# Kernel optimization log

Hardware: AMD Instinct MI355X
Metric: run time of the kernel (lower is better)

Reference implementation:

```python
import jax, jax.numpy as jnp
import numpy as np

N_NODES, N_EDGES, N_GRAPHS = 20000, 640000, 256
D_IN, H1, H2, H3, L, H4, ED = 7, 128, 128, 64, 16, 64, 1


def _gat_conv(x, src, dst, edge_attr, W, att_s, att_d, We, att_e, b):
    """PyG GATConv (heads=1, concat=True, edge_dim=ED, add_self_loops=True,
    fill_value='mean' for self-loop edge attrs, negative_slope=0.2)."""
    n = x.shape[0]
    h = x @ W                                  # [N, F]
    a_s = h @ att_s                            # [N]
    a_d = h @ att_d                            # [N]
    # append self loops; self-loop edge attr = mean of edge attrs
    loop = jnp.arange(n)
    src_f = jnp.concatenate([src, loop])
    dst_f = jnp.concatenate([dst, loop])
    ea_mean = edge_attr.mean(axis=0, keepdims=True)
    ea = jnp.concatenate([edge_attr, jnp.broadcast_to(ea_mean, (n, edge_attr.shape[1]))], axis=0)
    a_e = (ea @ We) @ att_e                    # [E+N]
    logits = jax.nn.leaky_relu(a_s[src_f] + a_d[dst_f] + a_e, 0.2)
    # neighborhood softmax over incoming edges of each dst node
    m = jax.ops.segment_max(logits, dst_f, num_segments=n)
    ex = jnp.exp(logits - m[dst_f])
    denom = jax.ops.segment_sum(ex, dst_f, num_segments=n)
    alpha = ex / denom[dst_f]                  # [E+N]
    out = jax.ops.segment_sum(alpha[:, None] * h[src_f], dst_f, num_segments=n)
    return out + b


def _branch(x, edge_index, edge_col, params):
    src, dst = edge_index[0], edge_index[1]
    for p in params:  # fixed 3 layers
        x = jax.nn.elu(_gat_conv(x, src, dst, edge_col, *p))
        # dropout p=0.2 is identity in eval mode
    return x


def _mean_pool(x, batch, num_graphs):
    s = jax.ops.segment_sum(x, batch, num_segments=num_graphs)
    cnt = jax.ops.segment_sum(jnp.ones((x.shape[0],), x.dtype), batch, num_segments=num_graphs)
    return s / jnp.maximum(cnt, 1.0)[:, None]


def setup_inputs() -> dict:
    key = jax.random.key(0)
    ks = jax.random.split(key, 40)
    inp = {
        "x1": jax.random.normal(ks[0], (N_NODES, D_IN), jnp.float32),
        "x2": jax.random.normal(ks[1], (N_NODES, D_IN), jnp.float32),
        "edge_index1": jax.random.randint(ks[2], (2, N_EDGES), 0, N_NODES),
        "edge_index2": jax.random.randint(ks[3], (2, N_EDGES), 0, N_NODES),
        "batch1": jnp.sort(jax.random.randint(ks[4], (N_NODES,), 0, N_GRAPHS)),
        "batch2": jnp.sort(jax.random.randint(ks[5], (N_NODES,), 0, N_GRAPHS)),
        "x_norm2_1": jax.random.normal(ks[6], (N_GRAPHS, L), jnp.float32),
        "x_norm2_2": jax.random.normal(ks[7], (N_GRAPHS, L), jnp.float32),
        "edge_col1": jax.random.normal(ks[8], (N_EDGES, ED), jnp.float32),
        "edge_col2": jax.random.normal(ks[9], (N_EDGES, ED), jnp.float32),
    }
    dims = [(D_IN, H1), (H1, H2), (H2, H3)]
    k = 10
    for i, (fi, fo) in enumerate(dims, start=1):
        sc = 1.0 / np.sqrt(fi)
        inp[f"W{i}"] = jax.random.normal(ks[k], (fi, fo), jnp.float32) * sc; k += 1
        inp[f"as{i}"] = jax.random.normal(ks[k], (fo,), jnp.float32) * 0.1; k += 1
        inp[f"ad{i}"] = jax.random.normal(ks[k], (fo,), jnp.float32) * 0.1; k += 1
        inp[f"We{i}"] = jax.random.normal(ks[k], (ED, fo), jnp.float32); k += 1
        inp[f"ae{i}"] = jax.random.normal(ks[k], (fo,), jnp.float32) * 0.1; k += 1
        inp[f"b{i}"] = jnp.zeros((fo,), jnp.float32); k += 1
    inp["linW"] = jax.random.normal(ks[k], (H3 + L, H4), jnp.float32) * (1.0 / np.sqrt(H3 + L)); k += 1
    inp["linb"] = jnp.zeros((H4,), jnp.float32)
    return inp


def reference(x1, x2, edge_index1, edge_index2, batch1, batch2, x_norm2_1, x_norm2_2,
              edge_col1, edge_col2,
              W1, as1, ad1, We1, ae1, b1,
              W2, as2, ad2, We2, ae2, b2,
              W3, as3, ad3, We3, ae3, b3,
              linW, linb):
    params = [(W1, as1, ad1, We1, ae1, b1),
              (W2, as2, ad2, We2, ae2, b2),
              (W3, as3, ad3, We3, ae3, b3)]
    h1 = _branch(x1, edge_index1, edge_col1, params)
    h2 = _branch(x2, edge_index2, edge_col2, params)
    g1 = _mean_pool(h1, batch1, N_GRAPHS)
    g2 = _mean_pool(h2, batch2, N_GRAPHS)
    o1 = jnp.concatenate([g1, x_norm2_1], axis=1) @ linW + linb
    o2 = jnp.concatenate([g2, x_norm2_2], axis=1) @ linW + linb
    return (o1, o2)
```

## Files before the change

kernel.cpp:

```cpp
#include <hip/hip_runtime.h>
#include <hip/hip_bf16.h>
#include <hip/hip_fp16.h>

#define N_NODES 20000
#define N_EDGES 640000
#define N_GRAPHS 256
#define NBUCK 313
#define NC 160
#define EPC 4000
#define DCAP 2560
#define CURP 16
#define STAGEN ((size_t)NBUCK*DCAP)

typedef short bf16v __attribute__((ext_vector_type(8)));
typedef float f32x4 __attribute__((ext_vector_type(4)));
typedef float f32x2 __attribute__((ext_vector_type(2)));

__device__ __forceinline__ float leaky02(float x){ return x > 0.f ? x : 0.2f*x; }
__device__ __forceinline__ float eluf(float x){ return x > 0.f ? x : (__expf(x) - 1.f); }
__device__ __forceinline__ unsigned short f2bf(float x){
  __hip_bfloat16 t = __float2bfloat16(x);
  return *reinterpret_cast<unsigned short*>(&t);
}
__device__ __forceinline__ float bflo(unsigned int u){ return __uint_as_float(u << 16); }
__device__ __forceinline__ float bfhi(unsigned int u){ return __uint_as_float(u & 0xffff0000u); }
__device__ __forceinline__ void pkfma(f32x2& acc, f32x2 a, f32x2 b){
  asm volatile("v_pk_fma_f32 %0, %1, %2, %0" : "+v"(acc) : "v"(a), "v"(b));
}

__global__ void init_kernel(int* __restrict__ bcur){
  int i = blockIdx.x*256 + threadIdx.x;
  if (i < 2*NBUCK){
    int b = i / NBUCK, j = i % NBUCK;
    bcur[((size_t)b*NBUCK + j)*CURP] = j*DCAP;
  }
}

__global__ __launch_bounds__(256) void binC_kernel(
    const int* __restrict__ ei0, const int* __restrict__ ei1,
    const float* __restrict__ ec0, const float* __restrict__ ec1,
    int* __restrict__ bcur, uint2* __restrict__ stage, float* __restrict__ part)
{
  int b = blockIdx.y;
  const int* srcp = (b ? ei1 : ei0);
  const int* dstp = srcp + N_EDGES;
  const float* ec = b ? ec1 : ec0;
  int* bcurb = bcur + (size_t)b*NBUCK*CURP;
  uint2* stageb = stage + (size_t)b*STAGEN;
  __shared__ uint2 recs[EPC];
  __shared__ int hist[NBUCK], rbase[NBUCK], rcur[NBUCK];
  int tid = threadIdx.x;
  for (int j = tid; j < NBUCK; j += 256){ hist[j] = 0; rcur[j] = 0; }
  __syncthreads();
  int e0 = blockIdx.x*EPC;
  float v = 0.f;
  for (int r = tid; r < EPC; r += 256){
    int i = e0 + r;
    int d = dstp[i];
    int bk = d >> 6;
    uint2 rec;
    rec.x = (unsigned)srcp[i] | ((unsigned)(d & 63) << 16);
    float e = ec[i];
    v += e;
    rec.y = ((unsigned)f2bf(e) << 16) | (unsigned)bk;
    recs[r] = rec;
    atomicAdd(&hist[bk], 1);
  }
  __syncthreads();
  for (int j = tid; j < NBUCK; j += 256){
    int h = hist[j];
    rbase[j] = h ? atomicAdd(&bcurb[j*CURP], h) : 0;
  }
  __syncthreads();
  for (int r = tid; r < EPC; r += 256){
    uint2 rc = recs[r];
    int bk = (int)(rc.y & 0xFFFFu);
    int p = rbase[bk] + atomicAdd(&rcur[bk], 1);
    if (p < (bk + 1)*DCAP) stageb[p] = rc;
  }
  for (int o = 32; o; o >>= 1) v += __shfl_down(v, o);
  __shared__ float wr[4];
  int lane = tid & 63, wv = tid >> 6;
  if (lane == 0) wr[wv] = v;
  __syncthreads();
  if (tid == 0) part[b*NC + blockIdx.x] = wr[0]+wr[1]+wr[2]+wr[3];
}

__global__ __launch_bounds__(512) void binB_kernel(
    const float* __restrict__ part,
    const int* __restrict__ bat0, const int* __restrict__ bat1,
    const float* __restrict__ We1, const float* __restrict__ ae1,
    const float* __restrict__ We2, const float* __restrict__ ae2,
    const float* __restrict__ We3, const float* __restrict__ ae3,
    int* __restrict__ gb, float* __restrict__ scal)
{
  int b = blockIdx.x;
  int tid = threadIdx.x;
  if (b == 0){
    int wv = tid >> 6, lane = tid & 63;
    if (wv < 3){
      const float* We = wv==0 ? We1 : (wv==1 ? We2 : We3);
      const float* ae = wv==0 ? ae1 : (wv==1 ? ae2 : ae3);
      int F = (wv==2) ? 64 : 128;
      float s = 0.f;
      for (int i = lane; i < F; i += 64) s += We[i]*ae[i];
      for (int o = 32; o; o >>= 1) s += __shfl_down(s, o);
      if (lane == 0) scal[2+wv] = s;
    }
  }
  {
    float s = 0.f;
    for (int i = tid; i < NC; i += 512) s += part[b*NC + i];
    for (int o = 32; o; o >>= 1) s += __shfl_down(s, o);
    __shared__ float fr[8];
    if ((tid & 63) == 0) fr[tid >> 6] = s;
    __syncthreads();
    if (tid == 0){
      float t = 0.f;
      for (int i = 0; i < 8; ++i) t += fr[i];
      scal[b] = t;
    }
  }
  {
    const int* batch = b ? bat1 : bat0;
    int* gbb = gb + b*257;
    if (tid <= N_GRAPHS){
      int g = tid, lo = 0, hi = N_NODES;
      while (lo < hi){ int mid = (lo+hi) >> 1; if (batch[mid] < g) lo = mid+1; else hi = mid; }
      gbb[g] = lo;
    }
  }
}

__global__ __launch_bounds__(256) void binD_kernel(
    const uint2* __restrict__ stage, const int* __restrict__ bcur,
    unsigned* __restrict__ final_, int2* __restrict__ rowp2)
{
  int b = blockIdx.y;
  int g = blockIdx.x;
  int tid = threadIdx.x;
  const uint2* stageb = stage + (size_t)b*STAGEN;
  unsigned* finb = final_ + (size_t)b*STAGEN;
  int2* rowb = rowp2 + (size_t)b*N_NODES;
  int cb = g*DCAP;
  int n = min(bcur[((size_t)b*NBUCK + g)*CURP] - cb, DCAP);
  __shared__ uint2 recs[DCAP];
  __shared__ int cnt64[64], cur64[64], off64[64];
  if (tid < 64) cnt64[tid] = 0;
  __syncthreads();
  for (int r = tid; r < n; r += 256){
    uint2 rc = stageb[cb + r];
    recs[r] = rc;
    atomicAdd(&cnt64[(rc.x >> 16) & 63], 1);
  }
  __syncthreads();
  if (tid == 0){
    int acc = 0;
    for (int dl = 0; dl < 64; ++dl){
      off64[dl] = acc; cur64[dl] = acc; acc += cnt64[dl];
    }
  }
  __syncthreads();
  int nd = min(64, N_NODES - g*64);
  if (tid < nd)
    rowb[g*64 + tid] = make_int2(cb + off64[tid], cb + off64[tid] + cnt64[tid]);
  for (int r = tid; r < n; r += 256){
    uint2 rc = recs[r];
    int dl = (rc.x >> 16) & 63;
    int p = atomicAdd(&cur64[dl], 1);
    finb[cb + p] = (rc.y & 0xFFFF0000u) | (rc.x & 0xFFFFu);
  }
}

template<int K, int F>
__global__ __launch_bounds__(256) void node_linear1_kernel(
    const float* __restrict__ x0, const float* __restrict__ x1,
    const float* __restrict__ W,
    const float* __restrict__ atts, const float* __restrict__ attd,
    unsigned short* __restrict__ hbAll, float* __restrict__ aSAll, float* __restrict__ aDAll)
{
  int b = blockIdx.y;
  const float* x = b ? x1 : x0;
  unsigned short* hb = hbAll + (size_t)b*N_NODES*128;
  float* a_s = aSAll + b*N_NODES;
  float* a_d = aDAll + b*N_NODES;
  constexpr int ROWS = 256 / F;
  __shared__ float Wl[K*F];
  __shared__ float xl[ROWS*K];
  __shared__ float swv[4], dwv[4];
  int tid = threadIdx.x;
  for (int i = tid; i < K*F; i += 256) Wl[i] = W[i];
  int f = tid % F;
  int lr = tid / F;
  float vs = atts[f], vd = attd[f];
  const int ntiles = (N_NODES + ROWS - 1)/ROWS;
  for (int t = blockIdx.x; t < ntiles; t += gridDim.x){
    int r0 = t*ROWS;
    __syncthreads();
    for (int i = tid; i < ROWS*K; i += 256){
      int r = i / K, k = i % K;
      int row = r0 + r;
      xl[i] = (row < N_NODES) ? x[row*K + k] : 0.f;
    }
    __syncthreads();
    float acc = 0.f;
    #pragma unroll
    for (int k = 0; k < K; ++k) acc += xl[lr*K + k] * Wl[k*F + f];
    int row = r0 + lr;
    if (row < N_NODES) hb[row*F + f] = f2bf(acc);
    float s = acc*vs, d = acc*vd;
    #pragma unroll
    for (int o = 32; o; o >>= 1){ s += __shfl_down(s, o); d += __shfl_down(d, o); }
    int wv = tid >> 6;
    if ((tid & 63) == 0){ swv[wv] = s; dwv[wv] = d; }
    __syncthreads();
    if (f == 0 && row < N_NODES){
      a_s[row] = swv[2*lr] + swv[2*lr+1];
      a_d[row] = dwv[2*lr] + dwv[2*lr+1];
    }
  }
}

template<int F>
__global__ __launch_bounds__(256) void gemm_mfma_kernel(
    const unsigned short* __restrict__ AAll, const float* __restrict__ W,
    const float* __restrict__ atts, const float* __restrict__ attd,
    unsigned short* __restrict__ hbAll, float* __restrict__ aSAll, float* __restrict__ aDAll)
{
  int b = blockIdx.y;
  const unsigned short* A = AAll + (size_t)b*N_NODES*128;
  unsigned short* hb = hbAll + (size_t)b*N_NODES*128;
  float* a_s = aSAll + b*N_NODES;
  float* a_d = aDAll + b*N_NODES;
  constexpr int NT = F/16;
  constexpr int KP = 136;
  __shared__ unsigned short Wb[F*KP];
  int tid = threadIdx.x;
  for (int idx = tid; idx < 128*F; idx += 256){
    int k = idx / F, col = idx % F;
    Wb[col*KP + k] = f2bf(W[idx]);
  }
  __syncthreads();
  int wave = tid >> 6, lane = tid & 63;
  int r0w = blockIdx.x*64 + wave*16;
  int arow = r0w + (lane & 15);
  bool av = arow < N_NODES;
  f32x4 acc[NT];
  #pragma unroll
  for (int nt = 0; nt < NT; ++nt) acc[nt] = 0.f;
  #pragma unroll
  for (int step = 0; step < 4; ++step){
    int kbase = step*32 + (lane>>4)*8;
    uint4 araw = av ? *reinterpret_cast<const uint4*>(&A[(size_t)arow*128 + kbase])
                    : make_uint4(0,0,0,0);
    bf16v af = __builtin_bit_cast(bf16v, araw);
    #pragma unroll
    for (int nt = 0; nt < NT; ++nt){
      uint4 braw = *reinterpret_cast<const uint4*>(&Wb[(nt*16 + (lane&15))*KP + kbase]);
      bf16v bfr = __builtin_bit_cast(bf16v, braw);
      acc[nt] = __builtin_amdgcn_mfma_f32_16x16x32_bf16(af, bfr, acc[nt], 0, 0, 0);
    }
  }
  float ps[4] = {0,0,0,0}, pd[4] = {0,0,0,0};
  #pragma unroll
  for (int nt = 0; nt < NT; ++nt){
    int col = nt*16 + (lane&15);
    float vs = atts[col], vd = attd[col];
    #pragma unroll
    for (int reg = 0; reg < 4; ++reg){
      int row = r0w + (lane>>4)*4 + reg;
      float v = acc[nt][reg];
      if (row < N_NODES) hb[(size_t)row*F + col] = f2bf(v);
      ps[reg] += v*vs;
      pd[reg] += v*vd;
    }
  }
  #pragma unroll
  for (int reg = 0; reg < 4; ++reg){
    float s = ps[reg], d = pd[reg];
    #pragma unroll
    for (int o = 1; o < 16; o <<= 1){ s += __shfl_xor(s, o); d += __shfl_xor(d, o); }
    int row = r0w + (lane>>4)*4 + reg;
    if ((lane & 15) == 0 && row < N_NODES){ a_s[row] = s; a_d[row] = d; }
  }
}

template<int F, bool W32>
__global__ __launch_bounds__(256) void aggregate_kernel(
    const unsigned short* __restrict__ hbAll,
    const float* __restrict__ aSAll, const float* __restrict__ aDAll,
    const unsigned* __restrict__ edgAll, const int2* __restrict__ rowp2All,
    const float* __restrict__ scal, int l,
    const float* __restrict__ bias,
    float* __restrict__ out32All, unsigned short* __restrict__ outbAll)
{
  constexpr int PERL = F/16;
  constexpr int PERH = PERL/2;
  constexpr int RSH = (F == 128) ? 8 : 7;
  constexpr int SUBB = (F == 128) ? 16 : 8;
  int bid = blockIdx.x;
  int b = bid & 1;
  const unsigned short* hb = hbAll + (size_t)b*N_NODES*128;
  const float* a_s = aSAll + b*N_NODES;
  const float* a_d = aDAll + b*N_NODES;
  const unsigned* edges = edgAll + (size_t)b*STAGEN;
  const int2* rowp2 = rowp2All + (size_t)b*N_NODES;
  __shared__ uint2 sp[4][64];
  int wv = threadIdx.x >> 6;
  int lane = threadIdx.x & 63;
  int d = (bid >> 1)*4 + wv;
  if (d >= N_NODES) return;
  int sub = lane & 15, grp = lane >> 4;
  const char* hb2 = (const char*)hb + sub*SUBB;
  float c = scal[2+l];
  float ae_self = (scal[b] * (1.0f/N_EDGES)) * c;
  float add_ = a_d[d];
  float p_self = __expf(fminf(leaky02(a_s[d] + add_ + ae_self), 60.f));
  float dsum = 0.f;
  f32x2 acc[PERH];
  #pragma unroll
  for (int i = 0; i < PERH; ++i) acc[i] = (f32x2){0.f, 0.f};
  if (grp == 0){
    f32x2 pself2 = {p_self, p_self};
    if (PERL == 8){
      uint4 q = *reinterpret_cast<const uint4*>(hb2 + ((unsigned)d << RSH));
      pkfma(acc[0], (f32x2){bflo(q.x), bfhi(q.x)}, pself2);
      pkfma(acc[1], (f32x2){bflo(q.y), bfhi(q.y)}, pself2);
      pkfma(acc[2], (f32x2){bflo(q.z), bfhi(q.z)}, pself2);
      pkfma(acc[3], (f32x2){bflo(q.w), bfhi(q.w)}, pself2);
    } else {
      uint2 q = *reinterpret_cast<const uint2*>(hb2 + ((unsigned)d << RSH));
      pkfma(acc[0], (f32x2){bflo(q.x), bfhi(q.x)}, pself2);
      pkfma(acc[1], (f32x2){bflo(q.y), bfhi(q.y)}, pself2);
    }
  }
  int2 r2 = rowp2[d];
  int e0 = r2.x, e1 = r2.y;
  for (int ch = e0; ch < e1; ch += 64){
    int n = min(64, e1 - ch);
    unsigned off0 = 0;
    float p0 = 0.f;
    if (lane < n){
      unsigned e = edges[ch + lane];
      unsigned s0 = e & 0xFFFFu;
      p0 = __expf(fminf(leaky02(a_s[s0] + add_ + c*bfhi(e)), 60.f));
      off0 = s0 << RSH;
    }
    dsum += p0;
    sp[wv][lane] = make_uint2(off0, __float_as_uint(p0));
    #pragma unroll 4
    for (int e4 = 0; e4 < n; e4 += 16){
      uint2 r0 = sp[wv][e4 + grp];
      uint2 r1 = sp[wv][e4 + 4 + grp];
      uint2 rr2 = sp[wv][e4 + 8 + grp];
      uint2 r3 = sp[wv][e4 + 12 + grp];
      f32x2 a0 = {__uint_as_float(r0.y), __uint_as_float(r0.y)};
      f32x2 a1 = {__uint_as_float(r1.y), __uint_as_float(r1.y)};
      f32x2 a2 = {__uint_as_float(rr2.y), __uint_as_float(rr2.y)};
      f32x2 a3 = {__uint_as_float(r3.y), __uint_as_float(r3.y)};
      if (PERL == 8){
        uint4 q0 = *reinterpret_cast<const uint4*>(hb2 + r0.x);
        uint4 q1 = *reinterpret_cast<const uint4*>(hb2 + r1.x);
        uint4 q2 = *reinterpret_cast<const uint4*>(hb2 + rr2.x);
        uint4 q3 = *reinterpret_cast<const uint4*>(hb2 + r3.x);
        pkfma(acc[0], (f32x2){bflo(q0.x), bfhi(q0.x)}, a0);
        pkfma(acc[1], (f32x2){bflo(q0.y), bfhi(q0.y)}, a0);
        pkfma(acc[2], (f32x2){bflo(q0.z), bfhi(q0.z)}, a0);
        pkfma(acc[3], (f32x2){bflo(q0.w), bfhi(q0.w)}, a0);
        pkfma(acc[0], (f32x2){bflo(q1.x), bfhi(q1.x)}, a1);
        pkfma(acc[1], (f32x2){bflo(q1.y), bfhi(q1.y)}, a1);
        pkfma(acc[2], (f32x2){bflo(q1.z), bfhi(q1.z)}, a1);
        pkfma(acc[3], (f32x2){bflo(q1.w), bfhi(q1.w)}, a1);
        pkfma(acc[0], (f32x2){bflo(q2.x), bfhi(q2.x)}, a2);
        pkfma(acc[1], (f32x2){bflo(q2.y), bfhi(q2.y)}, a2);
        pkfma(acc[2], (f32x2){bflo(q2.z), bfhi(q2.z)}, a2);
        pkfma(acc[3], (f32x2){bflo(q2.w), bfhi(q2.w)}, a2);
        pkfma(acc[0], (f32x2){bflo(q3.x), bfhi(q3.x)}, a3);
        pkfma(acc[1], (f32x2){bflo(q3.y), bfhi(q3.y)}, a3);
        pkfma(acc[2], (f32x2){bflo(q3.z), bfhi(q3.z)}, a3);
        pkfma(acc[3], (f32x2){bflo(q3.w), bfhi(q3.w)}, a3);
      } else {
        uint2 q0 = *reinterpret_cast<const uint2*>(hb2 + r0.x);
        uint2 q1 = *reinterpret_cast<const uint2*>(hb2 + r1.x);
        uint2 q2 = *reinterpret_cast<const uint2*>(hb2 + rr2.x);
        uint2 q3 = *reinterpret_cast<const uint2*>(hb2 + r3.x);
        pkfma(acc[0], (f32x2){bflo(q0.x), bfhi(q0.x)}, a0);
        pkfma(acc[1], (f32x2){bflo(q0.y), bfhi(q0.y)}, a0);
        pkfma(acc[0], (f32x2){bflo(q1.x), bfhi(q1.x)}, a1);
        pkfma(acc[1], (f32x2){bflo(q1.y), bfhi(q1.y)}, a1);
        pkfma(acc[0], (f32x2){bflo(q2.x), bfhi(q2.x)}, a2);
        pkfma(acc[1], (f32x2){bflo(q2.y), bfhi(q2.y)}, a2);
        pkfma(acc[0], (f32x2){bflo(q3.x), bfhi(q3.x)}, a3);
        pkfma(acc[1], (f32x2){bflo(q3.y), bfhi(q3.y)}, a3);
      }
    }
  }
  #pragma unroll
  for (int o = 32; o; o >>= 1) dsum += __shfl_xor(dsum, o);
  float denom = p_self + dsum;
  float inv = 1.0f/denom;
  float vv[PERL];
  #pragma unroll
  for (int i = 0; i < PERH; ++i){
    float v0 = acc[i].x, v1 = acc[i].y;
    v0 += __shfl_xor(v0, 16); v0 += __shfl_xor(v0, 32);
    v1 += __shfl_xor(v1, 16); v1 += __shfl_xor(v1, 32);
    vv[2*i]   = eluf(v0*inv + bias[PERL*sub + 2*i]);
    vv[2*i+1] = eluf(v1*inv + bias[PERL*sub + 2*i+1]);
  }
  if (grp == 0){
    if (W32){
      float* out32 = out32All + (size_t)b*N_NODES*64;
      *reinterpret_cast<float4*>(&out32[(size_t)d*64 + 4*sub]) = make_float4(vv[0],vv[1],vv[2],vv[3]);
    } else {
      unsigned short* outb = outbAll + (size_t)b*N_NODES*128;
      if (PERL == 8){
        uint4 o;
        o.x = (unsigned int)f2bf(vv[0]) | ((unsigned int)f2bf(vv[1]) << 16);
        o.y = (unsigned int)f2bf(vv[2]) | ((unsigned int)f2bf(vv[3]) << 16);
        o.z = (unsigned int)f2bf(vv[4]) | ((unsigned int)f2bf(vv[5]) << 16);
        o.w = (unsigned int)f2bf(vv[6]) | ((unsigned int)f2bf(vv[7]) << 16);
        *reinterpret_cast<uint4*>(&outb[(size_t)d*F + 8*sub]) = o;
      } else {
        uint2 o;
        o.x = (unsigned int)f2bf(vv[0]) | ((unsigned int)f2bf(vv[1]) << 16);
        o.y = (unsigned int)f2bf(vv[2]) | ((unsigned int)f2bf(vv[3]) << 16);
        *reinterpret_cast<uint2*>(&outb[(size_t)d*F + 4*sub]) = o;
      }
    }
  }
}

__global__ __launch_bounds__(256) void pool_final_kernel(
    const float* __restrict__ buf0, const int* __restrict__ gb,
    const float* __restrict__ xn0, const float* __restrict__ xn1,
    const float* __restrict__ linW, const float* __restrict__ linb,
    float* __restrict__ out)
{
  int bg = blockIdx.x;
  int b = bg >> 8, g = bg & 255;
  __shared__ float Wl[80*64];
  __shared__ float red[4][64];
  __shared__ float mf[64];
  int tid = threadIdx.x;
  for (int i = tid; i < 80*64; i += 256) Wl[i] = linW[i];
  const float* x = buf0 + (size_t)b*N_NODES*64;
  const int* gbb = gb + b*257;
  int s = gbb[g], e = gbb[g+1];
  int f = tid & 63, rg = tid >> 6;
  float acc = 0.f;
  for (int r = s + rg; r < e; r += 4) acc += x[r*64 + f];
  red[rg][f] = acc;
  __syncthreads();
  if (rg == 0)
    mf[f] = (red[0][f]+red[1][f]+red[2][f]+red[3][f]) / fmaxf((float)(e - s), 1.0f);
  __syncthreads();
  if (tid < 64){
    int j = tid;
    const float* xn = b ? xn1 : xn0;
    float a2 = linb[j];
    #pragma unroll 8
    for (int k = 0; k < 64; ++k) a2 += mf[k] * Wl[k*64 + j];
    #pragma unroll
    for (int k = 0; k < 16; ++k) a2 += xn[g*16+k] * Wl[(64+k)*64 + j];
    out[(size_t)(b*N_GRAPHS + g)*64 + j] = a2;
  }
}

extern "C" void kernel_launch(void* const* d_in, const int* in_sizes, int n_in,
                              void* d_out, int out_size, void* d_ws, size_t ws_size,
                              hipStream_t stream)
{
  const float* x1   = (const float*)d_in[0];
  const float* x2   = (const float*)d_in[1];
  const int*   ei1  = (const int*)d_in[2];
  const int*   ei2  = (const int*)d_in[3];
  const int*   bat1 = (const int*)d_in[4];
  const int*   bat2 = (const int*)d_in[5];
  const float* xn1  = (const float*)d_in[6];
  const float* xn2  = (const float*)d_in[7];
  const float* ec1  = (const float*)d_in[8];
  const float* ec2  = (const float*)d_in[9];
  const float* W[3]   = {(const float*)d_in[10], (const float*)d_in[16], (const float*)d_in[22]};
  const float* as_[3] = {(const float*)d_in[11], (const float*)d_in[17], (const float*)d_in[23]};
  const float* ad_[3] = {(const float*)d_in[12], (const float*)d_in[18], (const float*)d_in[24]};
  const float* We[3]  = {(const float*)d_in[13], (const float*)d_in[19], (const float*)d_in[25]};
  const float* ae[3]  = {(const float*)d_in[14], (const float*)d_in[20], (const float*)d_in[26]};
  const float* bb[3]  = {(const float*)d_in[15], (const float*)d_in[21], (const float*)d_in[27]};
  const float* linW = (const float*)d_in[28];
  const float* linb = (const float*)d_in[29];
  float* out = (float*)d_out;

  char* ws = (char*)d_ws;
  size_t off = 0;
  auto alloc = [&](size_t bytes)->char*{
    char* p = ws + off;
    off = (off + bytes + 255) & ~(size_t)255;
    return p;
  };
  unsigned short* hbA = (unsigned short*)alloc((size_t)2*N_NODES*128*2);
  unsigned short* hbB = (unsigned short*)alloc((size_t)2*N_NODES*128*2);
  float* buf0 = (float*)alloc((size_t)2*N_NODES*64*4);
  float* aS   = (float*)alloc((size_t)2*N_NODES*4);
  float* aD   = (float*)alloc((size_t)2*N_NODES*4);
  int* bcur   = (int*)alloc((size_t)2*NBUCK*CURP*4);
  int2* rowp2 = (int2*)alloc((size_t)2*N_NODES*8);
  uint2* stage = (uint2*)alloc((size_t)2*STAGEN*8);
  unsigned* final_ = (unsigned*)alloc((size_t)2*STAGEN*4);
  float* part = (float*)alloc((size_t)2*NC*4);
  int* gb     = (int*)alloc((size_t)2*257*4);
  float* scal = (float*)alloc(64);

  init_kernel<<<(2*NBUCK + 255)/256, 256, 0, stream>>>(bcur);
  binC_kernel<<<dim3(NC,2), 256, 0, stream>>>(ei1, ei2, ec1, ec2, bcur, stage, part);
  binB_kernel<<<2, 512, 0, stream>>>(part, bat1, bat2,
      We[0], ae[0], We[1], ae[1], We[2], ae[2], gb, scal);
  binD_kernel<<<dim3(NBUCK,2), 256, 0, stream>>>(stage, bcur, final_, rowp2);

  const int AGG = 2*(N_NODES/4);

  node_linear1_kernel<7,128><<<dim3(1024,2), 256, 0, stream>>>(
      x1, x2, W[0], as_[0], ad_[0], hbA, aS, aD);
  aggregate_kernel<128,false><<<AGG, 256, 0, stream>>>(
      hbA, aS, aD, final_, rowp2, scal, 0, bb[0], nullptr, hbB);

  gemm_mfma_kernel<128><<<dim3((N_NODES+63)/64,2), 256, 0, stream>>>(
      hbB, W[1], as_[1], ad_[1], hbA, aS, aD);
  aggregate_kernel<128,false><<<AGG, 256, 0, stream>>>(
      hbA, aS, aD, final_, rowp2, scal, 1, bb[1], nullptr, hbB);

  gemm_mfma_kernel<64><<<dim3((N_NODES+63)/64,2), 256, 0, stream>>>(
      hbB, W[2], as_[2], ad_[2], hbA, aS, aD);
  aggregate_kernel<64,true><<<AGG, 256, 0, stream>>>(
      hbA, aS, aD, final_, rowp2, scal, 2, bb[2], buf0, nullptr);

  pool_final_kernel<<<2*N_GRAPHS, 256, 0, stream>>>(
      buf0, gb, xn1, xn2, linW, linb, out);
}
```

Baseline: 200.0 us.

## Process two destination nodes per wavefront in GAT aggregation

Splits each 64-lane wavefront into two 32-lane halves, each aggregating its own destination node, and halves the grid size. Edge chunks become 32 wide, and the inner gather loop handles 8 edges per step with 2 lane groups per half instead of 4. With an average degree near 32 this is meant to cut idle lanes and raise work per wave. The cost is divergence when the two nodes have different degrees, since the loop runs to the larger of the two. Both halves share each wave's 64-entry shared-memory slot, and the reduction shuffles shrink to fit the 32-lane halves.

```diff
diff --git a/kernel.cpp b/kernel.cpp
--- a/kernel.cpp
+++ b/kernel.cpp
@@ -308,9 +308,10 @@
   __shared__ uint2 sp[4][64];
   int wv = threadIdx.x >> 6;
   int lane = threadIdx.x & 63;
-  int d = (bid >> 1)*4 + wv;
-  if (d >= N_NODES) return;
-  int sub = lane & 15, grp = lane >> 4;
+  int half = lane >> 5;
+  int hl = lane & 31;
+  int d = (bid >> 1)*8 + wv*2 + half;
+  int sub = hl & 15, grp = hl >> 4;
   const char* hb2 = (const char*)hb + sub*SUBB;
   float c = scal[2+l];
   float ae_self = (scal[b] * (1.0f/N_EDGES)) * c;
@@ -335,25 +336,28 @@
     }
   }
   int2 r2 = rowp2[d];
-  int e0 = r2.x, e1 = r2.y;
-  for (int ch = e0; ch < e1; ch += 64){
-    int n = min(64, e1 - ch);
+  int e0 = r2.x, deg = r2.y - r2.x;
+  int degmax = max(deg, __shfl_xor(deg, 32));
+  for (int ch = 0; ch < degmax; ch += 32){
+    int n = deg - ch;
     unsigned off0 = 0;
     float p0 = 0.f;
-    if (lane < n){
-      unsigned e = edges[ch + lane];
+    if (hl < n){
+      unsigned e = edges[e0 + ch + hl];
       unsigned s0 = e & 0xFFFFu;
       p0 = __expf(fminf(leaky02(a_s[s0] + add_ + c*bfhi(e)), 60.f));
       off0 = s0 << RSH;
     }
     dsum += p0;
     sp[wv][lane] = make_uint2(off0, __float_as_uint(p0));
+    int nmax = min(32, degmax - ch);
     #pragma unroll 4
-    for (int e4 = 0; e4 < n; e4 += 16){
-      uint2 r0 = sp[wv][e4 + grp];
-      uint2 r1 = sp[wv][e4 + 4 + grp];
-      uint2 rr2 = sp[wv][e4 + 8 + grp];
-      uint2 r3 = sp[wv][e4 + 12 + grp];
+    for (int e8 = 0; e8 < nmax; e8 += 8){
+      int base = half*32 + e8 + grp;
+      uint2 r0 = sp[wv][base];
+      uint2 r1 = sp[wv][base + 2];
+      uint2 rr2 = sp[wv][base + 4];
+      uint2 r3 = sp[wv][base + 6];
       f32x2 a0 = {__uint_as_float(r0.y), __uint_as_float(r0.y)};
       f32x2 a1 = {__uint_as_float(r1.y), __uint_as_float(r1.y)};
       f32x2 a2 = {__uint_as_float(rr2.y), __uint_as_float(rr2.y)};
@@ -396,15 +400,15 @@
     }
   }
   #pragma unroll
-  for (int o = 32; o; o >>= 1) dsum += __shfl_xor(dsum, o);
+  for (int o = 16; o; o >>= 1) dsum += __shfl_xor(dsum, o);
   float denom = p_self + dsum;
   float inv = 1.0f/denom;
   float vv[PERL];
   #pragma unroll
   for (int i = 0; i < PERH; ++i){
     float v0 = acc[i].x, v1 = acc[i].y;
-    v0 += __shfl_xor(v0, 16); v0 += __shfl_xor(v0, 32);
-    v1 += __shfl_xor(v1, 16); v1 += __shfl_xor(v1, 32);
+    v0 += __shfl_xor(v0, 16);
+    v1 += __shfl_xor(v1, 16);
     vv[2*i]   = eluf(v0*inv + bias[PERL*sub + 2*i]);
     vv[2*i+1] = eluf(v1*inv + bias[PERL*sub + 2*i+1]);
   }
@@ -517,7 +521,7 @@
       We[0], ae[0], We[1], ae[1], We[2], ae[2], gb, scal);
   binD_kernel<<<dim3(NBUCK,2), 256, 0, stream>>>(stage, bcur, final_, rowp2);
 
-  const int AGG = 2*(N_NODES/4);
+  const int AGG = 2*(N_NODES/8);
 
   node_linear1_kernel<7,128><<<dim3(1024,2), 256, 0, stream>>>(
       x1, x2, W[0], as_[0], ad_[0], hbA, aS, aD);
```

Result: faster. 188.4 us (-5.8%).
